# Kernel tuning notes

Hardware: AMD Instinct MI355X
Metric: run time of the kernel (lower is better)

## Reference

```python
import jax, jax.numpy as jnp
import numpy as np

NUM_GROUPS = 32


def setup_inputs() -> dict:
    key = jax.random.key(0)
    x = jax.random.normal(key, (16384, 4096), dtype=jnp.float32)
    return {"x": x}


def reference(x):
    N, D = x.shape
    G = NUM_GROUPS
    d = D // G
    # [N, G, d] -> mean-center over batch
    xg = x.reshape(N, G, d)
    xg = xg - xg.mean(axis=0, keepdims=True)
    # [G, N, d]
    xg = jnp.transpose(xg, (1, 0, 2))
    # per-group covariance: [G, d, d]
    covs = jnp.einsum('gnd,gne->gde', xg, xg) / (N - 1)
    S, U = jnp.linalg.eigh(covs)  # S: [G, d], U: [G, d, d]
    # whitening transform W = U diag(S^-1/2) U^T : [G, d, d]
    W = jnp.einsum('gde,ge,gfe->gdf', U, jax.lax.rsqrt(S), U)
    out = jnp.einsum('gnd,gdf->gnf', xg, W)  # [G, N, d]
    return jnp.transpose(out, (1, 0, 2)).reshape(N, D)
```

## Files before the change

kernel.cpp:

```cpp
#include <hip/hip_runtime.h>
#include <cstddef>

#define NROWS 16384
#define NCOLS 4096
#define NG 32
#define GD 128
#define NPC 16

typedef float f32x4 __attribute__((ext_vector_type(4)));
typedef short bf16x8 __attribute__((ext_vector_type(8)));

__device__ inline unsigned short f2bf(float f) {
    unsigned int u = __builtin_bit_cast(unsigned int, f);
    u += 0x7fffu + ((u >> 16) & 1u);
    return (unsigned short)(u >> 16);
}

__global__ __launch_bounds__(256) void k_cov(
    const float* __restrict__ x, float* __restrict__ xtx, float* __restrict__ ps)
{
    __shared__ unsigned short xt[2][128][42];
    __shared__ float red[4][128];
    const int bid = blockIdx.x;
    const int g = bid >> 4, p = bid & 15;
    const int t = threadIdx.x;
    const int f2 = t & 63;
    const int w = t >> 6;
    const int lane = t & 63;
    const int lm = lane & 15, lk = lane >> 4;
    const float* xb = x + (size_t)(p * 1024) * NCOLS + g * GD + 2 * f2;

    float csum0 = 0.f, csum1 = 0.f;
    f32x4 acc[2][8];
#pragma unroll
    for (int mi = 0; mi < 2; ++mi)
#pragma unroll
        for (int ni = 0; ni < 8; ++ni) acc[mi][ni] = (f32x4){0.f, 0.f, 0.f, 0.f};

    float2 v[8];
#define CLOAD(CC) \
    _Pragma("unroll") for (int i = 0; i < 8; ++i) \
        v[i] = *(const float2*)(xb + (size_t)((CC) * 32 + w * 8 + i) * NCOLS);
#define CWRITE(BUF) { \
    bf16x8 h0, h1; \
    _Pragma("unroll") for (int i = 0; i < 8; ++i) { \
        csum0 += v[i].x; csum1 += v[i].y; \
        h0[i] = (short)f2bf(v[i].x); h1[i] = (short)f2bf(v[i].y); } \
    *(bf16x8*)&xt[BUF][2 * f2][w * 8] = h0; \
    *(bf16x8*)&xt[BUF][2 * f2 + 1][w * 8] = h1; }

    CLOAD(0);
    CWRITE(0);
    __syncthreads();

    for (int c = 0; c < 32; ++c) {
        const int cur = c & 1;
        if (c < 31) { CLOAD(c + 1); }
        bf16x8 A0 = *(const bf16x8*)&xt[cur][w * 32 + lm][lk * 8];
        bf16x8 A1 = *(const bf16x8*)&xt[cur][w * 32 + 16 + lm][lk * 8];
        bf16x8 B[8];
#pragma unroll
        for (int n = 0; n < 8; ++n)
            B[n] = *(const bf16x8*)&xt[cur][n * 16 + lm][lk * 8];
#pragma unroll
        for (int n = 0; n < 8; ++n) {
            acc[0][n] = __builtin_amdgcn_mfma_f32_16x16x32_bf16(A0, B[n], acc[0][n], 0, 0, 0);
            acc[1][n] = __builtin_amdgcn_mfma_f32_16x16x32_bf16(A1, B[n], acc[1][n], 0, 0, 0);
        }
        if (c < 31) { CWRITE(cur ^ 1); }
        __syncthreads();
    }
#undef CLOAD
#undef CWRITE

    float* ob = xtx + (size_t)bid * (GD * GD);
#pragma unroll
    for (int mi = 0; mi < 2; ++mi)
#pragma unroll
        for (int ni = 0; ni < 8; ++ni) {
            const int i0 = w * 32 + mi * 16 + lk * 4;
            const int j = ni * 16 + lm;
#pragma unroll
            for (int r = 0; r < 4; ++r)
                ob[(size_t)(i0 + r) * GD + j] = acc[mi][ni][r];
        }
    red[w][2 * f2] = csum0;
    red[w][2 * f2 + 1] = csum1;
    __syncthreads();
    if (t < 128) {
        float s = 0.f;
#pragma unroll
        for (int r = 0; r < 4; ++r) s += red[r][t];
        ps[(size_t)bid * GD + t] = s;
    }
}

__global__ __launch_bounds__(256) void k_mean(
    const float* __restrict__ ps, float* __restrict__ mean)
{
    const int col = blockIdx.x * 256 + threadIdx.x;
    const int g = col >> 7, d = col & 127;
    float s = 0.f;
#pragma unroll
    for (int p = 0; p < NPC; ++p) s += ps[(size_t)(g * NPC + p) * GD + d];
    mean[col] = s * (1.0f / (float)NROWS);
}

__global__ __launch_bounds__(256) void k_covreduce(
    const float* __restrict__ xtx, const float* __restrict__ mean,
    float* __restrict__ C)
{
    __shared__ float mu[128];
    const int bid = blockIdx.x;
    const int g = bid >> 4, s = bid & 15;
    const int t = threadIdx.x;
    if (t < 128) mu[t] = mean[g * GD + t];
    __syncthreads();
    const int e = s * 1024 + t * 4;
    const int i = e >> 7, j = e & 127;
    float4 sum = make_float4(0.f, 0.f, 0.f, 0.f);
#pragma unroll
    for (int p = 0; p < NPC; ++p) {
        const float4 vv = *(const float4*)(xtx + ((size_t)(g * NPC + p) << 14) + e);
        sum.x += vv.x; sum.y += vv.y; sum.z += vv.z; sum.w += vv.w;
    }
    const float inv = 1.0f / (float)(NROWS - 1);
    const float mi2 = (float)NROWS * mu[i];
    float4 r;
    r.x = (sum.x - mi2 * mu[j + 0]) * inv;
    r.y = (sum.y - mi2 * mu[j + 1]) * inv;
    r.z = (sum.z - mi2 * mu[j + 2]) * inv;
    r.w = (sum.w - mi2 * mu[j + 3]) * inv;
    *(float4*)(C + (size_t)g * (GD * GD) + e) = r;
}

__global__ __launch_bounds__(256) void k_prep(
    const float* __restrict__ Cg, float* __restrict__ scale,
    float* __restrict__ Y0, float* __restrict__ Z0)
{
    __shared__ float Cs[128][129];
    __shared__ float rs[128];
    __shared__ float sinv[1];
    const int g = blockIdx.x;
    const int t = threadIdx.x;
    for (int k = 0; k < 64; ++k) {
        int e = t + 256 * k;
        Cs[e >> 7][e & 127] = Cg[(size_t)g * (GD * GD) + e];
    }
    __syncthreads();
    if (t < 128) {
        float s = 0.f;
        for (int i = 0; i < 128; ++i) s += fabsf(Cs[i][t]);
        rs[t] = s;
    }
    __syncthreads();
    if (t == 0) {
        float up = 0.f, lo = 1e30f;
        for (int i = 0; i < 128; ++i) {
            up = fmaxf(up, rs[i]);
            lo = fminf(lo, 2.0f * Cs[i][i] - rs[i]);
        }
        float c = 0.5f * (up + fmaxf(lo, 0.0f));
        c = fmaxf(c, 1e-20f);
        sinv[0] = 1.0f / c;
        scale[g] = rsqrtf(c);
    }
    __syncthreads();
    const float invc = sinv[0];
    for (int k = 0; k < 64; ++k) {
        int e = t + 256 * k;
        int i = e >> 7, j = e & 127;
        Y0[(size_t)g * (GD * GD) + e] = Cs[i][j] * invc;
        Z0[(size_t)g * (GD * GD) + e] = (i == j) ? 1.0f : 0.0f;
    }
}

__global__ __launch_bounds__(256) void k_ns_iter(
    const float* __restrict__ Yin, const float* __restrict__ Zin,
    float* __restrict__ Yout, float* __restrict__ Zout)
{
    __shared__ float Ys[128][132];
    __shared__ float Zs[128][132];
    __shared__ float Ts[128][16];
    const int bid = blockIdx.x;
    const int g = bid >> 3;
    const int sl = bid & 7;
    const int J0 = sl * 16;
    const int t = threadIdx.x;
    const float* Yg = Yin + (size_t)g * GD * GD;
    const float* Zg = Zin + (size_t)g * GD * GD;
#pragma unroll
    for (int k = 0; k < 16; ++k) {
        int q = t + 256 * k;
        int row = q >> 5, c4 = q & 31;
        *(float4*)&Ys[row][c4 * 4] = *(const float4*)(Yg + (size_t)q * 4);
        *(float4*)&Zs[row][c4 * 4] = *(const float4*)(Zg + (size_t)q * 4);
    }
    __syncthreads();
    const int i = t >> 1;
    const int jb = (t & 1) * 8;

    float accT[8];
#pragma unroll
    for (int q = 0; q < 8; ++q) accT[q] = 0.f;
    for (int k4 = 0; k4 < 32; ++k4) {
        float4 zv = *(const float4*)&Zs[i][k4 * 4];
        float zz[4] = {zv.x, zv.y, zv.z, zv.w};
#pragma unroll
        for (int e = 0; e < 4; ++e) {
            const int k = k4 * 4 + e;
            float4 y0 = *(const float4*)&Ys[k][J0 + jb];
            float4 y1 = *(const float4*)&Ys[k][J0 + jb + 4];
            float yy[8] = {y0.x, y0.y, y0.z, y0.w, y1.x, y1.y, y1.z, y1.w};
#pragma unroll
            for (int q = 0; q < 8; ++q) accT[q] = fmaf(zz[e], yy[q], accT[q]);
        }
    }
#pragma unroll
    for (int q = 0; q < 8; ++q) Ts[i][jb + q] = accT[q];
    __syncthreads();

    float ay[8], az[8];
#pragma unroll
    for (int q = 0; q < 8; ++q) { ay[q] = 0.f; az[q] = 0.f; }
    for (int k4 = 0; k4 < 32; ++k4) {
        float4 yv = *(const float4*)&Ys[i][k4 * 4];
        float4 zv = *(const float4*)&Zs[i][k4 * 4];
        float yy[4] = {yv.x, yv.y, yv.z, yv.w};
        float zz[4] = {zv.x, zv.y, zv.z, zv.w};
#pragma unroll
        for (int e = 0; e < 4; ++e) {
            const int k = k4 * 4 + e;
            float4 t0 = *(const float4*)&Ts[k][jb];
            float4 t1 = *(const float4*)&Ts[k][jb + 4];
            float tt[8] = {t0.x, t0.y, t0.z, t0.w, t1.x, t1.y, t1.z, t1.w};
#pragma unroll
            for (int q = 0; q < 8; ++q) {
                ay[q] = fmaf(yy[e], tt[q], ay[q]);
                az[q] = fmaf(zz[e], tt[q], az[q]);
            }
        }
    }
    float4 yc0 = *(const float4*)&Ys[i][J0 + jb];
    float4 yc1 = *(const float4*)&Ys[i][J0 + jb + 4];
    float4 zc0 = *(const float4*)&Zs[i][J0 + jb];
    float4 zc1 = *(const float4*)&Zs[i][J0 + jb + 4];
    float* Yo = Yout + (size_t)g * GD * GD + (size_t)i * GD + J0 + jb;
    float* Zo = Zout + (size_t)g * GD * GD + (size_t)i * GD + J0 + jb;
    *(float4*)(Yo)     = make_float4(1.5f*yc0.x - 0.5f*ay[0], 1.5f*yc0.y - 0.5f*ay[1],
                                     1.5f*yc0.z - 0.5f*ay[2], 1.5f*yc0.w - 0.5f*ay[3]);
    *(float4*)(Yo + 4) = make_float4(1.5f*yc1.x - 0.5f*ay[4], 1.5f*yc1.y - 0.5f*ay[5],
                                     1.5f*yc1.z - 0.5f*ay[6], 1.5f*yc1.w - 0.5f*ay[7]);
    *(float4*)(Zo)     = make_float4(1.5f*zc0.x - 0.5f*az[0], 1.5f*zc0.y - 0.5f*az[1],
                                     1.5f*zc0.z - 0.5f*az[2], 1.5f*zc0.w - 0.5f*az[3]);
    *(float4*)(Zo + 4) = make_float4(1.5f*zc1.x - 0.5f*az[4], 1.5f*zc1.y - 0.5f*az[5],
                                     1.5f*zc1.z - 0.5f*az[6], 1.5f*zc1.w - 0.5f*az[7]);
}

__global__ __launch_bounds__(256) void k_wprep(
    const float* __restrict__ Z, const float* __restrict__ scale,
    const float* __restrict__ mean,
    unsigned short* __restrict__ WT, float* __restrict__ muW)
{
    __shared__ float Zs[128][129];
    __shared__ float mu[128];
    const int g = blockIdx.x;
    const int t = threadIdx.x;
    const float sc = scale[g];
    if (t < 128) mu[t] = mean[g * GD + t];
    for (int k = 0; k < 64; ++k) {
        int e = t + 256 * k;
        Zs[e >> 7][e & 127] = Z[(size_t)g * (GD * GD) + e];
    }
    __syncthreads();
    const int n = t & 127, kh = t >> 7;
    unsigned short* o = WT + (size_t)g * (GD * GD) + (size_t)n * GD + kh * 64;
    for (int k = 0; k < 64; k += 2) {
        unsigned int pk = (unsigned int)f2bf(Zs[kh * 64 + k][n] * sc)
                        | ((unsigned int)f2bf(Zs[kh * 64 + k + 1][n] * sc) << 16);
        *(unsigned int*)(o + k) = pk;
    }
    if (t < 128) {
        float s = 0.f;
        for (int d = 0; d < 128; ++d) s = fmaf(mu[d], Zs[d][t], s);
        muW[g * GD + t] = s * sc;
    }
}

__global__ __launch_bounds__(256) void k_apply(
    const float* __restrict__ x, const unsigned short* __restrict__ WT,
    const float* __restrict__ muW, float* __restrict__ out)
{
    const int bid = blockIdx.x;
    const int g = bid >> 6, rbo = bid & 63;
    const int t = threadIdx.x;
    const int lane = t & 63, w = t >> 6;
    const int lm = lane & 15, lk = lane >> 4;
    const int nh = w >> 1;
    const int m0w = (w & 1) * 32;

    bf16x8 Wf[4][4];
    {
        const unsigned short* wg = WT + (size_t)g * (GD * GD);
#pragma unroll
        for (int ni = 0; ni < 4; ++ni)
#pragma unroll
            for (int ks = 0; ks < 4; ++ks)
                Wf[ni][ks] = *(const bf16x8*)(wg
                    + (size_t)(nh * 64 + ni * 16 + lm) * GD + ks * 32 + lk * 8);
    }
    float mw[4];
#pragma unroll
    for (int ni = 0; ni < 4; ++ni) mw[ni] = muW[g * GD + nh * 64 + ni * 16 + lm];

    float4 uA[16], uB[16];

#define ALD(U, C) { \
    const float* ab_ = x + (size_t)(rbo * 256 + (C) * 64 + m0w) * NCOLS + g * GD; \
    _Pragma("unroll") for (int ks = 0; ks < 4; ++ks) { \
        const float* p0_ = ab_ + (size_t)lm * NCOLS + ks * 32 + lk * 8; \
        U[ks * 4 + 0] = *(const float4*)(p0_); \
        U[ks * 4 + 1] = *(const float4*)(p0_ + 4); \
        U[ks * 4 + 2] = *(const float4*)(p0_ + (size_t)16 * NCOLS); \
        U[ks * 4 + 3] = *(const float4*)(p0_ + (size_t)16 * NCOLS + 4); } }

#define ACS(U, C) { \
    f32x4 acc[2][4]; \
    _Pragma("unroll") for (int mi = 0; mi < 2; ++mi) \
        _Pragma("unroll") for (int ni = 0; ni < 4; ++ni) \
            acc[mi][ni] = (f32x4){0.f, 0.f, 0.f, 0.f}; \
    _Pragma("unroll") for (int ks = 0; ks < 4; ++ks) { \
        float4 q0 = U[ks * 4 + 0], q1 = U[ks * 4 + 1]; \
        float4 q2 = U[ks * 4 + 2], q3 = U[ks * 4 + 3]; \
        bf16x8 a0, a1; \
        a0[0] = (short)f2bf(q0.x); a0[1] = (short)f2bf(q0.y); \
        a0[2] = (short)f2bf(q0.z); a0[3] = (short)f2bf(q0.w); \
        a0[4] = (short)f2bf(q1.x); a0[5] = (short)f2bf(q1.y); \
        a0[6] = (short)f2bf(q1.z); a0[7] = (short)f2bf(q1.w); \
        a1[0] = (short)f2bf(q2.x); a1[1] = (short)f2bf(q2.y); \
        a1[2] = (short)f2bf(q2.z); a1[3] = (short)f2bf(q2.w); \
        a1[4] = (short)f2bf(q3.x); a1[5] = (short)f2bf(q3.y); \
        a1[6] = (short)f2bf(q3.z); a1[7] = (short)f2bf(q3.w); \
        _Pragma("unroll") for (int ni = 0; ni < 4; ++ni) { \
            acc[0][ni] = __builtin_amdgcn_mfma_f32_16x16x32_bf16(a0, Wf[ni][ks], acc[0][ni], 0, 0, 0); \
            acc[1][ni] = __builtin_amdgcn_mfma_f32_16x16x32_bf16(a1, Wf[ni][ks], acc[1][ni], 0, 0, 0); } } \
    float* ob_ = out + (size_t)(rbo * 256 + (C) * 64 + m0w) * NCOLS + g * GD + nh * 64; \
    _Pragma("unroll") for (int mi = 0; mi < 2; ++mi) \
        _Pragma("unroll") for (int ni = 0; ni < 4; ++ni) \
            _Pragma("unroll") for (int r = 0; r < 4; ++r) \
                __builtin_nontemporal_store( \
                    acc[mi][ni][r] - mw[ni], \
                    ob_ + (size_t)(mi * 16 + lk * 4 + r) * NCOLS + ni * 16 + lm); }

    ALD(uA, 0);
    ALD(uB, 1);
    ACS(uA, 0);
    ALD(uA, 2);
    ACS(uB, 1);
    ALD(uB, 3);
    ACS(uA, 2);
    ACS(uB, 3);
#undef ALD
#undef ACS
}

extern "C" void kernel_launch(void* const* d_in, const int* in_sizes, int n_in,
                              void* d_out, int out_size, void* d_ws, size_t ws_size,
                              hipStream_t stream) {
    const float* x = (const float*)d_in[0];
    float* out = (float*)d_out;
    float* ws = (float*)d_ws;

    float* xtx   = ws;
    float* ps    = xtx + (size_t)NG * NPC * GD * GD;
    float* mean  = ps + (size_t)NG * NPC * GD;
    float* scale = mean + NCOLS;
    float* Cbuf  = scale + 32;
    float* Ya    = Cbuf + (size_t)NG * GD * GD;
    float* Za    = Ya + (size_t)NG * GD * GD;
    float* Yb    = Za + (size_t)NG * GD * GD;
    float* Zb    = Yb + (size_t)NG * GD * GD;
    float* muW   = Zb + (size_t)NG * GD * GD;
    unsigned short* WT = (unsigned short*)(muW + NCOLS);

    k_cov<<<NG * NPC, 256, 0, stream>>>(x, xtx, ps);
    k_mean<<<NCOLS / 256, 256, 0, stream>>>(ps, mean);
    k_covreduce<<<NG * NPC, 256, 0, stream>>>(xtx, mean, Cbuf);
    k_prep<<<NG, 256, 0, stream>>>(Cbuf, scale, Ya, Za);
    for (int it = 0; it < 6; ++it) {
        if ((it & 1) == 0)
            k_ns_iter<<<NG * 8, 256, 0, stream>>>(Ya, Za, Yb, Zb);
        else
            k_ns_iter<<<NG * 8, 256, 0, stream>>>(Yb, Zb, Ya, Za);
    }
    k_wprep<<<NG, 256, 0, stream>>>(Za, scale, mean, WT, muW);
    k_apply<<<NG * 64, 256, 0, stream>>>(x, WT, muW, out);
}
```

Baseline: 380.7 us.

## Cache bf16 copy of x from covariance pass and reuse it in apply

The covariance kernel now also writes its bf16-converted x tile to a workspace buffer laid out group-major. The apply kernel reads this compact bf16 buffer instead of re-reading and re-converting fp32 x, which halves the bytes it reads and drops the conversion work there. In exchange, k_cov does extra global stores (128 MB of bf16), and the apply kernel's explicit double-buffered prefetch is replaced by a simple loop.

```diff
diff --git a/kernel.cpp b/kernel.cpp
--- a/kernel.cpp
+++ b/kernel.cpp
@@ -17,7 +17,8 @@
 }
 
 __global__ __launch_bounds__(256) void k_cov(
-    const float* __restrict__ x, float* __restrict__ xtx, float* __restrict__ ps)
+    const float* __restrict__ x, float* __restrict__ xtx, float* __restrict__ ps,
+    unsigned short* __restrict__ xhi)
 {
     __shared__ unsigned short xt[2][128][42];
     __shared__ float red[4][128];
@@ -29,6 +30,8 @@
     const int lane = t & 63;
     const int lm = lane & 15, lk = lane >> 4;
     const float* xb = x + (size_t)(p * 1024) * NCOLS + g * GD + 2 * f2;
+    unsigned int* xo = (unsigned int*)(xhi
+        + ((size_t)g * NROWS + p * 1024 + w * 8) * GD + 2 * f2);
 
     float csum0 = 0.f, csum1 = 0.f;
     f32x4 acc[2][8];
@@ -41,16 +44,18 @@
 #define CLOAD(CC) \
     _Pragma("unroll") for (int i = 0; i < 8; ++i) \
         v[i] = *(const float2*)(xb + (size_t)((CC) * 32 + w * 8 + i) * NCOLS);
-#define CWRITE(BUF) { \
+#define CWRITE(BUF, CC) { \
     bf16x8 h0, h1; \
     _Pragma("unroll") for (int i = 0; i < 8; ++i) { \
         csum0 += v[i].x; csum1 += v[i].y; \
-        h0[i] = (short)f2bf(v[i].x); h1[i] = (short)f2bf(v[i].y); } \
+        unsigned int b0 = f2bf(v[i].x), b1 = f2bf(v[i].y); \
+        h0[i] = (short)b0; h1[i] = (short)b1; \
+        xo[(size_t)((CC) * 32 + i) * 64] = b0 | (b1 << 16); } \
     *(bf16x8*)&xt[BUF][2 * f2][w * 8] = h0; \
     *(bf16x8*)&xt[BUF][2 * f2 + 1][w * 8] = h1; }
 
     CLOAD(0);
-    CWRITE(0);
+    CWRITE(0, 0);
     __syncthreads();
 
     for (int c = 0; c < 32; ++c) {
@@ -67,7 +72,7 @@
             acc[0][n] = __builtin_amdgcn_mfma_f32_16x16x32_bf16(A0, B[n], acc[0][n], 0, 0, 0);
             acc[1][n] = __builtin_amdgcn_mfma_f32_16x16x32_bf16(A1, B[n], acc[1][n], 0, 0, 0);
         }
-        if (c < 31) { CWRITE(cur ^ 1); }
+        if (c < 31) { CWRITE(cur ^ 1, c + 1); }
         __syncthreads();
     }
 #undef CLOAD
@@ -288,7 +293,7 @@
 }
 
 __global__ __launch_bounds__(256) void k_apply(
-    const float* __restrict__ x, const unsigned short* __restrict__ WT,
+    const unsigned short* __restrict__ xhi, const unsigned short* __restrict__ WT,
     const float* __restrict__ muW, float* __restrict__ out)
 {
     const int bid = blockIdx.x;
@@ -313,55 +318,46 @@
 #pragma unroll
     for (int ni = 0; ni < 4; ++ni) mw[ni] = muW[g * GD + nh * 64 + ni * 16 + lm];
 
-    float4 uA[16], uB[16];
-
-#define ALD(U, C) { \
-    const float* ab_ = x + (size_t)(rbo * 256 + (C) * 64 + m0w) * NCOLS + g * GD; \
-    _Pragma("unroll") for (int ks = 0; ks < 4; ++ks) { \
-        const float* p0_ = ab_ + (size_t)lm * NCOLS + ks * 32 + lk * 8; \
-        U[ks * 4 + 0] = *(const float4*)(p0_); \
-        U[ks * 4 + 1] = *(const float4*)(p0_ + 4); \
-        U[ks * 4 + 2] = *(const float4*)(p0_ + (size_t)16 * NCOLS); \
-        U[ks * 4 + 3] = *(const float4*)(p0_ + (size_t)16 * NCOLS + 4); } }
-
-#define ACS(U, C) { \
-    f32x4 acc[2][4]; \
-    _Pragma("unroll") for (int mi = 0; mi < 2; ++mi) \
-        _Pragma("unroll") for (int ni = 0; ni < 4; ++ni) \
-            acc[mi][ni] = (f32x4){0.f, 0.f, 0.f, 0.f}; \
-    _Pragma("unroll") for (int ks = 0; ks < 4; ++ks) { \
-        float4 q0 = U[ks * 4 + 0], q1 = U[ks * 4 + 1]; \
-        float4 q2 = U[ks * 4 + 2], q3 = U[ks * 4 + 3]; \
-        bf16x8 a0, a1; \
-        a0[0] = (short)f2bf(q0.x); a0[1] = (short)f2bf(q0.y); \
-        a0[2] = (short)f2bf(q0.z); a0[3] = (short)f2bf(q0.w); \
-        a0[4] = (short)f2bf(q1.x); a0[5] = (short)f2bf(q1.y); \
-        a0[6] = (short)f2bf(q1.z); a0[7] = (short)f2bf(q1.w); \
-        a1[0] = (short)f2bf(q2.x); a1[1] = (short)f2bf(q2.y); \
-        a1[2] = (short)f2bf(q2.z); a1[3] = (short)f2bf(q2.w); \
-        a1[4] = (short)f2bf(q3.x); a1[5] = (short)f2bf(q3.y); \
-        a1[6] = (short)f2bf(q3.z); a1[7] = (short)f2bf(q3.w); \
-        _Pragma("unroll") for (int ni = 0; ni < 4; ++ni) { \
-            acc[0][ni] = __builtin_amdgcn_mfma_f32_16x16x32_bf16(a0, Wf[ni][ks], acc[0][ni], 0, 0, 0); \
-            acc[1][ni] = __builtin_amdgcn_mfma_f32_16x16x32_bf16(a1, Wf[ni][ks], acc[1][ni], 0, 0, 0); } } \
-    float* ob_ = out + (size_t)(rbo * 256 + (C) * 64 + m0w) * NCOLS + g * GD + nh * 64; \
-    _Pragma("unroll") for (int mi = 0; mi < 2; ++mi) \
-        _Pragma("unroll") for (int ni = 0; ni < 4; ++ni) \
-            _Pragma("unroll") for (int r = 0; r < 4; ++r) \
-                __builtin_nontemporal_store( \
-                    acc[mi][ni][r] - mw[ni], \
-                    ob_ + (size_t)(mi * 16 + lk * 4 + r) * NCOLS + ni * 16 + lm); }
-
-    ALD(uA, 0);
-    ALD(uB, 1);
-    ACS(uA, 0);
-    ALD(uA, 2);
-    ACS(uB, 1);
-    ALD(uB, 3);
-    ACS(uA, 2);
-    ACS(uB, 3);
-#undef ALD
-#undef ACS
+    for (int c = 0; c < 4; ++c) {
+        const int row0 = rbo * 256 + c * 64;
+        const unsigned short* ab = xhi
+            + ((size_t)g * NROWS + row0 + m0w + lm) * GD + lk * 8;
+
+        bf16x8 u[8];
+#pragma unroll
+        for (int ks = 0; ks < 4; ++ks) {
+            u[ks * 2 + 0] = *(const bf16x8*)(ab + ks * 32);
+            u[ks * 2 + 1] = *(const bf16x8*)(ab + (size_t)16 * GD + ks * 32);
+        }
+
+        f32x4 acc[2][4];
+#pragma unroll
+        for (int mi = 0; mi < 2; ++mi)
+#pragma unroll
+            for (int ni = 0; ni < 4; ++ni) acc[mi][ni] = (f32x4){0.f, 0.f, 0.f, 0.f};
+
+#pragma unroll
+        for (int ks = 0; ks < 4; ++ks) {
+#pragma unroll
+            for (int ni = 0; ni < 4; ++ni) {
+                acc[0][ni] = __builtin_amdgcn_mfma_f32_16x16x32_bf16(
+                    u[ks * 2 + 0], Wf[ni][ks], acc[0][ni], 0, 0, 0);
+                acc[1][ni] = __builtin_amdgcn_mfma_f32_16x16x32_bf16(
+                    u[ks * 2 + 1], Wf[ni][ks], acc[1][ni], 0, 0, 0);
+            }
+        }
+
+        float* ob = out + (size_t)(row0 + m0w) * NCOLS + g * GD + nh * 64;
+#pragma unroll
+        for (int mi = 0; mi < 2; ++mi)
+#pragma unroll
+            for (int ni = 0; ni < 4; ++ni)
+#pragma unroll
+                for (int r = 0; r < 4; ++r)
+                    __builtin_nontemporal_store(
+                        acc[mi][ni][r] - mw[ni],
+                        ob + (size_t)(mi * 16 + lk * 4 + r) * NCOLS + ni * 16 + lm);
+    }
 }
 
 extern "C" void kernel_launch(void* const* d_in, const int* in_sizes, int n_in,
@@ -381,9 +377,10 @@
     float* Yb    = Za + (size_t)NG * GD * GD;
     float* Zb    = Yb + (size_t)NG * GD * GD;
     float* muW   = Zb + (size_t)NG * GD * GD;
-    unsigned short* WT = (unsigned short*)(muW + NCOLS);
-
-    k_cov<<<NG * NPC, 256, 0, stream>>>(x, xtx, ps);
+    unsigned short* WT  = (unsigned short*)(muW + NCOLS);
+    unsigned short* xhi = WT + (size_t)NG * GD * GD;
+
+    k_cov<<<NG * NPC, 256, 0, stream>>>(x, xtx, ps, xhi);
     k_mean<<<NCOLS / 256, 256, 0, stream>>>(ps, mean);
     k_covreduce<<<NG * NPC, 256, 0, stream>>>(xtx, mean, Cbuf);
     k_prep<<<NG, 256, 0, stream>>>(Cbuf, scale, Ya, Za);
@@ -394,5 +391,5 @@
             k_ns_iter<<<NG * 8, 256, 0, stream>>>(Yb, Zb, Ya, Za);
     }
     k_wprep<<<NG, 256, 0, stream>>>(Za, scale, mean, WT, muW);
-    k_apply<<<NG * 64, 256, 0, stream>>>(x, WT, muW, out);
-}
+    k_apply<<<NG * 64, 256, 0, stream>>>(xhi, WT, muW, out);
+}
```

Result: faster. 353.4 us (-7.2%).
